# Optimization experiments

Hardware: AMD Instinct MI355X
Metric: run time of the kernel (lower is better)

The kernel has to match this reference:

```python
import jax, jax.numpy as jnp
import numpy as np
from jax import lax

H = 128  # hidden_size


def lstm_last_h(x, w_ih, w_hh, b_ih, b_hh):
    """PyTorch-style single-layer LSTM; returns final hidden state.
    x: (B, T, D). Gate order i, f, g, o. w_ih: (4H, D), w_hh: (4H, H)."""
    B = x.shape[0]
    Hh = w_hh.shape[1]
    x_proj = jnp.einsum('btd,gd->btg', x, w_ih) + b_ih + b_hh  # (B, T, 4H)

    def step(carry, xt):
        h, c = carry
        gates = xt + h @ w_hh.T
        i, f, g, o = jnp.split(gates, 4, axis=-1)
        i = jax.nn.sigmoid(i)
        f = jax.nn.sigmoid(f)
        g = jnp.tanh(g)
        o = jax.nn.sigmoid(o)
        c = f * c + i * g
        h = o * jnp.tanh(c)
        return (h, c), None

    init = (jnp.zeros((B, Hh), x.dtype), jnp.zeros((B, Hh), x.dtype))
    (h, _), _ = lax.scan(step, init, jnp.swapaxes(x_proj, 0, 1))
    return h  # (B, H)


def setup_inputs() -> dict:
    key = jax.random.key(0)
    ks = jax.random.split(key, 12)
    s = 0.05
    return {
        'x_players': jax.random.normal(ks[0], (64, 22, 128, 2), jnp.float32),
        'x_ball': jax.random.normal(ks[1], (64, 128, 2), jnp.float32),
        'p_w_ih': jax.random.normal(ks[2], (4 * H, 2), jnp.float32) * s,
        'p_w_hh': jax.random.normal(ks[3], (4 * H, H), jnp.float32) * s,
        'p_b_ih': jax.random.normal(ks[4], (4 * H,), jnp.float32) * s,
        'p_b_hh': jax.random.normal(ks[5], (4 * H,), jnp.float32) * s,
        'b_w_ih': jax.random.normal(ks[6], (4 * H, 2), jnp.float32) * s,
        'b_w_hh': jax.random.normal(ks[7], (4 * H, H), jnp.float32) * s,
        'b_b_ih': jax.random.normal(ks[8], (4 * H,), jnp.float32) * s,
        'b_b_hh': jax.random.normal(ks[9], (4 * H,), jnp.float32) * s,
        'fc_w': jax.random.normal(ks[10], (40, 2 * H), jnp.float32) * s,
        'fc_b': jax.random.normal(ks[11], (40,), jnp.float32) * s,
    }


def reference(x_players, x_ball, p_w_ih, p_w_hh, p_b_ih, p_b_hh,
              b_w_ih, b_w_hh, b_b_ih, b_b_hh, fc_w, fc_b):
    B, P, T, D = x_players.shape
    ball_h = lstm_last_h(x_ball, b_w_ih, b_w_hh, b_b_ih, b_b_hh)  # (B, H)
    # Shared player LSTM: fold players into batch (replaces per-player loop).
    ph = lstm_last_h(x_players.reshape(B * P, T, D),
                     p_w_ih, p_w_hh, p_b_ih, p_b_hh).reshape(B, P, H)
    ball_rep = jnp.broadcast_to(ball_h[:, None, :], (B, P, H))
    combined = jnp.concatenate([ph, ball_rep], axis=-1)  # (B, P, 2H)
    out = combined @ fc_w.T + fc_b  # (B, P, 40)
    return out.reshape(B, P, 20, 2)
```

## Files before the change

kernel.cpp:

```cpp
#include <hip/hip_runtime.h>


#define HDIM 128
#define TSTEPS 128
#define NPLAYER 1408
#define NSEQ 1472
#define NB 8
#define NBLK (NSEQ / NB)
#define NPBLK (NPLAYER / NB)
#define KT 5
#define BSTR 168
#define XSTR 258

typedef _Float16 f16x8 __attribute__((ext_vector_type(8)));
typedef _Float16 f16x2 __attribute__((ext_vector_type(2)));
typedef float    f32x4 __attribute__((ext_vector_type(4)));

#define LOG2E 1.44269504f

__device__ __forceinline__ float rcp_fast(float x) { return __builtin_amdgcn_rcpf(x); }
__device__ __forceinline__ float sigmoid_f(float x) {
    return rcp_fast(1.0f + __builtin_amdgcn_exp2f(-LOG2E * x));
}
__device__ __forceinline__ float tanh_f(float x) {
    return 1.0f - 2.0f * rcp_fast(__builtin_amdgcn_exp2f(2.0f * LOG2E * x) + 1.0f);
}
__device__ __forceinline__ float dpp_xor8(float x) {
    return __int_as_float(__builtin_amdgcn_update_dpp(
        __float_as_int(x), __float_as_int(x), 0x128 , 0xF, 0xF, false));
}

__global__ void __launch_bounds__(512)
__attribute__((amdgpu_waves_per_eu(2, 2)))
lstm_kernel(const float* __restrict__ x_players, const float* __restrict__ x_ball,
            const float* __restrict__ p_w_ih, const float* __restrict__ p_w_hh,
            const float* __restrict__ p_b_ih, const float* __restrict__ p_b_hh,
            const float* __restrict__ b_w_ih, const float* __restrict__ b_w_hh,
            const float* __restrict__ b_b_ih, const float* __restrict__ b_b_hh,
            float* __restrict__ h_all)
{
    const int tid  = threadIdx.x;
    const int blk  = blockIdx.x;
    const int w    = tid >> 6;
    const int lane = tid & 63;
    const int nn   = lane & 15;
    const int q    = lane >> 4;

    const bool ball = (blk >= NPBLK);
    const float* w_ih = ball ? b_w_ih : p_w_ih;
    const float* w_hh = ball ? b_w_hh : p_w_hh;
    const float* bih  = ball ? b_b_ih : p_b_ih;
    const float* bhh  = ball ? b_b_hh : p_b_hh;
    const float* xg   = ball ? (x_ball    + (size_t)(blk - NPBLK) * NB * TSTEPS * 2)
                             : (x_players + (size_t)blk * NB * TSTEPS * 2);

    __shared__ __align__(16) _Float16 b_sh[2][NB * BSTR];
    __shared__ __align__(16) float x_sh[NB * XSTR];

    for (int i = tid; i < NB * 256; i += 512)
        x_sh[(i >> 8) * XSTR + (i & 255)] = xg[i];
    for (int i = tid; i < 2 * NB * BSTR / 2; i += 512)
        ((int*)b_sh)[i] = 0;

    f16x8 afr[4][KT];
    #pragma unroll
    for (int mi = 0; mi < 4; ++mi) {
        const int r = mi * HDIM + w * 16 + nn;
        const float* wr = w_hh + (size_t)r * HDIM;
        #pragma unroll
        for (int kt = 0; kt < 4; ++kt) {
            const float* p = wr + kt * 32 + q * 8;
            f16x8 a8;
            #pragma unroll
            for (int j = 0; j < 8; ++j) a8[j] = (_Float16)p[j];
            afr[mi][kt] = a8;
        }
        f16x8 a8 = {};
        if (q == 0) {
            a8[0] = (_Float16)w_ih[2 * r];
            a8[1] = (_Float16)w_ih[2 * r + 1];
            a8[2] = (_Float16)(bih[r] + bhh[r]);
        }
        afr[mi][4] = a8;
    }

    const int colh   = nn & 7;
    const int rowoff = (nn < 8) ? 0 : 2;
    const int hrow   = w * 16 + 4 * q + rowoff;
    float c0 = 0.f, c1 = 0.f;
    float h0 = 0.f, h1 = 0.f;

    __syncthreads();
    if (tid < NB) {
        _Float16* br0 = &b_sh[0][tid * BSTR];
        br0[128] = (_Float16)x_sh[tid * XSTR];
        br0[129] = (_Float16)x_sh[tid * XSTR + 1];
        br0[130] = (_Float16)1.0f;
        b_sh[1][tid * BSTR + 130] = (_Float16)1.0f;
    }
    __syncthreads();

    f16x8 bfr[KT] = {};

    auto substep = [&](int s, const _Float16* bc, _Float16* bn, bool last) {
        if (nn < 8) {
            #pragma unroll
            for (int kt = 0; kt < KT; ++kt)
                bfr[kt] = *(const f16x8*)(bc + nn * BSTR + kt * 32 + q * 8);
        }

        f32x4 acc[4];
        #pragma unroll
        for (int mi = 0; mi < 4; ++mi) acc[mi] = (f32x4){0.f, 0.f, 0.f, 0.f};
        #pragma unroll
        for (int kt = 0; kt < KT; ++kt)
            #pragma unroll
            for (int mi = 0; mi < 4; ++mi)
                acc[mi] = __builtin_amdgcn_mfma_f32_16x16x32_f16(afr[mi][kt], bfr[kt], acc[mi], 0, 0, 0);

        if (!last && tid < NB) {
            const float x0 = x_sh[tid * XSTR + 2 * (s + 1)];
            const float x1 = x_sh[tid * XSTR + 2 * (s + 1) + 1];
            *(f16x2*)&bn[tid * BSTR + 128] = (f16x2){(_Float16)x0, (_Float16)x1};
        }

        float u0[4], u1[4];
        #pragma unroll
        for (int mi = 0; mi < 4; ++mi) {
            const float r2 = dpp_xor8(acc[mi][2]);
            const float r3 = dpp_xor8(acc[mi][3]);
            u0[mi] = (nn < 8) ? acc[mi][0] : r2;
            u1[mi] = (nn < 8) ? acc[mi][1] : r3;
        }
        const float i0 = sigmoid_f(u0[0]), i1 = sigmoid_f(u1[0]);
        const float f0 = sigmoid_f(u0[1]), f1 = sigmoid_f(u1[1]);
        const float g0 = tanh_f(u0[2]),    g1 = tanh_f(u1[2]);
        const float o0 = sigmoid_f(u0[3]), o1 = sigmoid_f(u1[3]);
        c0 = __builtin_fmaf(f0, c0, i0 * g0);
        c1 = __builtin_fmaf(f1, c1, i1 * g1);
        h0 = o0 * tanh_f(c0);
        h1 = o1 * tanh_f(c1);

        if (!last) {
            *(f16x2*)&bn[colh * BSTR + hrow] = (f16x2){(_Float16)h0, (_Float16)h1};
            __syncthreads();
        }
    };

    _Float16* b0 = &b_sh[0][0];
    _Float16* b1 = &b_sh[1][0];
    #pragma unroll 1
    for (int it = 0; it < TSTEPS / 2 - 1; ++it) {
        substep(2 * it,     b0, b1, false);
        substep(2 * it + 1, b1, b0, false);
        asm volatile("" :
            "+a"(afr[0][0]), "+a"(afr[0][1]), "+a"(afr[0][2]), "+a"(afr[0][3]), "+a"(afr[0][4]),
            "+a"(afr[1][0]), "+a"(afr[1][1]), "+a"(afr[1][2]), "+a"(afr[1][3]), "+a"(afr[1][4]),
            "+a"(afr[2][0]), "+a"(afr[2][1]), "+a"(afr[2][2]), "+a"(afr[2][3]), "+a"(afr[2][4]),
            "+a"(afr[3][0]), "+a"(afr[3][1]), "+a"(afr[3][2]), "+a"(afr[3][3]), "+a"(afr[3][4]));
    }
    substep(126, b0, b1, false);
    substep(127, b1, b0, true);

    float* hp = h_all + (size_t)(blk * NB + colh) * HDIM + hrow;
    hp[0] = h0; hp[1] = h1;
}

__global__ void __launch_bounds__(256)
fc_kernel(const float* __restrict__ h_all, const float* __restrict__ fc_w,
          const float* __restrict__ fc_b, float* __restrict__ out)
{
    const int blk = blockIdx.x;
    const int tid = threadIdx.x;

    __shared__ __align__(16) float comb[8][2 * HDIM];
    for (int i = tid; i < 8 * HDIM; i += 256) {
        const int p = i >> 7, off = i & 127;
        const int gp = 8 * blk + p;
        comb[p][off]        = h_all[(size_t)gp * HDIM + off];
        comb[p][HDIM + off] = h_all[(size_t)(NPLAYER + gp / 22) * HDIM + off];
    }
    __syncthreads();

    for (int o = tid; o < 8 * 40; o += 256) {
        const int p = o / 40, row = o - p * 40;
        const float* wr = fc_w + (size_t)row * 2 * HDIM;
        const float* cp = &comb[p][0];
        float a0 = fc_b[row], a1 = 0.f, a2 = 0.f, a3 = 0.f;
        #pragma unroll
        for (int k = 0; k < 2 * HDIM; k += 4) {
            float4 wv = *(const float4*)(wr + k);
            float4 cv = *(const float4*)(cp + k);
            a0 = __builtin_fmaf(wv.x, cv.x, a0);
            a1 = __builtin_fmaf(wv.y, cv.y, a1);
            a2 = __builtin_fmaf(wv.z, cv.z, a2);
            a3 = __builtin_fmaf(wv.w, cv.w, a3);
        }
        out[(size_t)(8 * blk + p) * 40 + row] = (a0 + a1) + (a2 + a3);
    }
}

extern "C" void kernel_launch(void* const* d_in, const int* in_sizes, int n_in,
                              void* d_out, int out_size, void* d_ws, size_t ws_size,
                              hipStream_t stream) {
    const float* x_players = (const float*)d_in[0];
    const float* x_ball    = (const float*)d_in[1];
    const float* p_w_ih    = (const float*)d_in[2];
    const float* p_w_hh    = (const float*)d_in[3];
    const float* p_b_ih    = (const float*)d_in[4];
    const float* p_b_hh    = (const float*)d_in[5];
    const float* b_w_ih    = (const float*)d_in[6];
    const float* b_w_hh    = (const float*)d_in[7];
    const float* b_b_ih    = (const float*)d_in[8];
    const float* b_b_hh    = (const float*)d_in[9];
    const float* fc_w      = (const float*)d_in[10];
    const float* fc_b      = (const float*)d_in[11];

    float* h_all = (float*)d_ws;

    lstm_kernel<<<dim3(NBLK), dim3(512), 0, stream>>>(
        x_players, x_ball, p_w_ih, p_w_hh, p_b_ih, p_b_hh,
        b_w_ih, b_w_hh, b_b_ih, b_b_hh, h_all);

    fc_kernel<<<dim3(NPBLK), dim3(256), 0, stream>>>(
        h_all, fc_w, fc_b, (float*)d_out);
}
```

Before: 185.4 us.

## Halve LSTM sequences per block and use 4-wave blocks covering 32 hidden rows each

Each block now handles 4 sequences with 256 threads instead of 8 with 512, so there are twice as many blocks (368) to fill the GPU's compute units. Each wave now owns 32 hidden rows (8 MFMA tiles) and recombines gate outputs with an extra ds_swizzle xor-4 exchange. The bias/input tile is issued first against a zero accumulator rather than zero-initializing. This doubles weight register footprint per wave and wastes more of the MFMA's 16 columns (only 4 valid), but shortens per-step barrier scope and raises occupancy.

```diff
diff --git a/kernel.cpp b/kernel.cpp
--- a/kernel.cpp
+++ b/kernel.cpp
@@ -5,7 +5,7 @@
 #define TSTEPS 128
 #define NPLAYER 1408
 #define NSEQ 1472
-#define NB 8
+#define NB 4
 #define NBLK (NSEQ / NB)
 #define NPBLK (NPLAYER / NB)
 #define KT 5
@@ -27,10 +27,13 @@
 }
 __device__ __forceinline__ float dpp_xor8(float x) {
     return __int_as_float(__builtin_amdgcn_update_dpp(
-        __float_as_int(x), __float_as_int(x), 0x128 , 0xF, 0xF, false));
-}
-
-__global__ void __launch_bounds__(512)
+        __float_as_int(x), __float_as_int(x), 0x128, 0xF, 0xF, false));
+}
+__device__ __forceinline__ float swz_xor4(float x) {
+    return __int_as_float(__builtin_amdgcn_ds_swizzle(__float_as_int(x), 0x101F));
+}
+
+__global__ void __launch_bounds__(256)
 __attribute__((amdgpu_waves_per_eu(2, 2)))
 lstm_kernel(const float* __restrict__ x_players, const float* __restrict__ x_ball,
             const float* __restrict__ p_w_ih, const float* __restrict__ p_w_hh,
@@ -45,6 +48,8 @@
     const int lane = tid & 63;
     const int nn   = lane & 15;
     const int q    = lane >> 4;
+    const int bit2 = (nn >> 2) & 1;
+    const int bit3 = (nn >> 3) & 1;
 
     const bool ball = (blk >= NPBLK);
     const float* w_ih = ball ? b_w_ih : p_w_ih;
@@ -57,38 +62,42 @@
     __shared__ __align__(16) _Float16 b_sh[2][NB * BSTR];
     __shared__ __align__(16) float x_sh[NB * XSTR];
 
-    for (int i = tid; i < NB * 256; i += 512)
+    for (int i = tid; i < NB * 256; i += 256)
         x_sh[(i >> 8) * XSTR + (i & 255)] = xg[i];
-    for (int i = tid; i < 2 * NB * BSTR / 2; i += 512)
+    for (int i = tid; i < 2 * NB * BSTR / 2; i += 256)
         ((int*)b_sh)[i] = 0;
 
-    f16x8 afr[4][KT];
+    f16x8 afr[8][KT];
     #pragma unroll
-    for (int mi = 0; mi < 4; ++mi) {
-        const int r = mi * HDIM + w * 16 + nn;
-        const float* wr = w_hh + (size_t)r * HDIM;
-        #pragma unroll
-        for (int kt = 0; kt < 4; ++kt) {
-            const float* p = wr + kt * 32 + q * 8;
-            f16x8 a8;
+    for (int g = 0; g < 4; ++g)
+        #pragma unroll
+        for (int hh = 0; hh < 2; ++hh) {
+            const int mi = 2 * g + hh;
+            const int r  = g * HDIM + w * 32 + hh * 16 + nn;
+            const float* wr = w_hh + (size_t)r * HDIM;
             #pragma unroll
-            for (int j = 0; j < 8; ++j) a8[j] = (_Float16)p[j];
-            afr[mi][kt] = a8;
-        }
-        f16x8 a8 = {};
-        if (q == 0) {
-            a8[0] = (_Float16)w_ih[2 * r];
-            a8[1] = (_Float16)w_ih[2 * r + 1];
-            a8[2] = (_Float16)(bih[r] + bhh[r]);
-        }
-        afr[mi][4] = a8;
-    }
-
-    const int colh   = nn & 7;
-    const int rowoff = (nn < 8) ? 0 : 2;
-    const int hrow   = w * 16 + 4 * q + rowoff;
-    float c0 = 0.f, c1 = 0.f;
-    float h0 = 0.f, h1 = 0.f;
+            for (int kt = 0; kt < 4; ++kt) {
+                const float* p = wr + kt * 32 + q * 8;
+                f16x8 a8;
+                #pragma unroll
+                for (int j = 0; j < 8; ++j) a8[j] = (_Float16)p[j];
+                afr[mi][kt] = a8;
+            }
+            f16x8 a8 = {};
+            if (q == 0) {
+                a8[0] = (_Float16)w_ih[2 * r];
+                a8[1] = (_Float16)w_ih[2 * r + 1];
+                a8[2] = (_Float16)(bih[r] + bhh[r]);
+            }
+            afr[mi][4] = a8;
+        }
+
+    const int colh = nn & 3;
+    const int r0   = w * 32 + bit2 * 16 + q * 4 + bit3 * 2;
+    float c0 = 0.f, c1 = 0.f, h0 = 0.f, h1 = 0.f;
+
+    f32x4 zero4 = (f32x4){0.f, 0.f, 0.f, 0.f};
+    asm volatile("" : "+v"(zero4));
 
     __syncthreads();
     if (tid < NB) {
@@ -103,19 +112,20 @@
     f16x8 bfr[KT] = {};
 
     auto substep = [&](int s, const _Float16* bc, _Float16* bn, bool last) {
-        if (nn < 8) {
+        if (nn < NB) {
             #pragma unroll
             for (int kt = 0; kt < KT; ++kt)
                 bfr[kt] = *(const f16x8*)(bc + nn * BSTR + kt * 32 + q * 8);
         }
 
-        f32x4 acc[4];
-        #pragma unroll
-        for (int mi = 0; mi < 4; ++mi) acc[mi] = (f32x4){0.f, 0.f, 0.f, 0.f};
-        #pragma unroll
-        for (int kt = 0; kt < KT; ++kt)
+        f32x4 acc[8];
+        #pragma unroll
+        for (int mi = 0; mi < 8; ++mi)
+            acc[mi] = __builtin_amdgcn_mfma_f32_16x16x32_f16(afr[mi][4], bfr[4], zero4, 0, 0, 0);
+        #pragma unroll
+        for (int kt = 0; kt < 4; ++kt)
             #pragma unroll
-            for (int mi = 0; mi < 4; ++mi)
+            for (int mi = 0; mi < 8; ++mi)
                 acc[mi] = __builtin_amdgcn_mfma_f32_16x16x32_f16(afr[mi][kt], bfr[kt], acc[mi], 0, 0, 0);
 
         if (!last && tid < NB) {
@@ -124,25 +134,34 @@
             *(f16x2*)&bn[tid * BSTR + 128] = (f16x2){(_Float16)x0, (_Float16)x1};
         }
 
-        float u0[4], u1[4];
-        #pragma unroll
-        for (int mi = 0; mi < 4; ++mi) {
+        float u[8][2];
+        #pragma unroll
+        for (int mi = 0; mi < 8; ++mi) {
             const float r2 = dpp_xor8(acc[mi][2]);
             const float r3 = dpp_xor8(acc[mi][3]);
-            u0[mi] = (nn < 8) ? acc[mi][0] : r2;
-            u1[mi] = (nn < 8) ? acc[mi][1] : r3;
-        }
-        const float i0 = sigmoid_f(u0[0]), i1 = sigmoid_f(u1[0]);
-        const float f0 = sigmoid_f(u0[1]), f1 = sigmoid_f(u1[1]);
-        const float g0 = tanh_f(u0[2]),    g1 = tanh_f(u1[2]);
-        const float o0 = sigmoid_f(u0[3]), o1 = sigmoid_f(u1[3]);
+            u[mi][0] = bit3 ? r2 : acc[mi][0];
+            u[mi][1] = bit3 ? r3 : acc[mi][1];
+        }
+        float v[4][2];
+        #pragma unroll
+        for (int g = 0; g < 4; ++g) {
+            const float p0 = swz_xor4(u[2 * g + 1][0]);
+            const float p1 = swz_xor4(u[2 * g + 1][1]);
+            v[g][0] = bit2 ? p0 : u[2 * g][0];
+            v[g][1] = bit2 ? p1 : u[2 * g][1];
+        }
+
+        const float i0 = sigmoid_f(v[0][0]), i1 = sigmoid_f(v[0][1]);
+        const float f0 = sigmoid_f(v[1][0]), f1 = sigmoid_f(v[1][1]);
+        const float g0 = tanh_f(v[2][0]),    g1 = tanh_f(v[2][1]);
+        const float o0 = sigmoid_f(v[3][0]), o1 = sigmoid_f(v[3][1]);
         c0 = __builtin_fmaf(f0, c0, i0 * g0);
         c1 = __builtin_fmaf(f1, c1, i1 * g1);
         h0 = o0 * tanh_f(c0);
         h1 = o1 * tanh_f(c1);
 
         if (!last) {
-            *(f16x2*)&bn[colh * BSTR + hrow] = (f16x2){(_Float16)h0, (_Float16)h1};
+            *(f16x2*)&bn[colh * BSTR + r0] = (f16x2){(_Float16)h0, (_Float16)h1};
             __syncthreads();
         }
     };
@@ -153,16 +172,20 @@
     for (int it = 0; it < TSTEPS / 2 - 1; ++it) {
         substep(2 * it,     b0, b1, false);
         substep(2 * it + 1, b1, b0, false);
-        asm volatile("" :
-            "+a"(afr[0][0]), "+a"(afr[0][1]), "+a"(afr[0][2]), "+a"(afr[0][3]), "+a"(afr[0][4]),
-            "+a"(afr[1][0]), "+a"(afr[1][1]), "+a"(afr[1][2]), "+a"(afr[1][3]), "+a"(afr[1][4]),
-            "+a"(afr[2][0]), "+a"(afr[2][1]), "+a"(afr[2][2]), "+a"(afr[2][3]), "+a"(afr[2][4]),
-            "+a"(afr[3][0]), "+a"(afr[3][1]), "+a"(afr[3][2]), "+a"(afr[3][3]), "+a"(afr[3][4]));
+        asm volatile("" : "+a"(afr[0][0]), "+a"(afr[0][1]), "+a"(afr[0][2]), "+a"(afr[0][3]), "+a"(afr[0][4]));
+        asm volatile("" : "+a"(afr[1][0]), "+a"(afr[1][1]), "+a"(afr[1][2]), "+a"(afr[1][3]), "+a"(afr[1][4]));
+        asm volatile("" : "+a"(afr[2][0]), "+a"(afr[2][1]), "+a"(afr[2][2]), "+a"(afr[2][3]), "+a"(afr[2][4]));
+        asm volatile("" : "+a"(afr[3][0]), "+a"(afr[3][1]), "+a"(afr[3][2]), "+a"(afr[3][3]), "+a"(afr[3][4]));
+        asm volatile("" : "+a"(afr[4][0]), "+a"(afr[4][1]), "+a"(afr[4][2]), "+a"(afr[4][3]), "+a"(afr[4][4]));
+        asm volatile("" : "+a"(afr[5][0]), "+a"(afr[5][1]), "+a"(afr[5][2]), "+a"(afr[5][3]), "+a"(afr[5][4]));
+        asm volatile("" : "+a"(afr[6][0]), "+a"(afr[6][1]), "+a"(afr[6][2]), "+a"(afr[6][3]), "+a"(afr[6][4]));
+        asm volatile("" : "+a"(afr[7][0]), "+a"(afr[7][1]), "+a"(afr[7][2]), "+a"(afr[7][3]), "+a"(afr[7][4]));
+        asm volatile("" : "+v"(zero4));
     }
     substep(126, b0, b1, false);
     substep(127, b1, b0, true);
 
-    float* hp = h_all + (size_t)(blk * NB + colh) * HDIM + hrow;
+    float* hp = h_all + (size_t)(blk * NB + colh) * HDIM + r0;
     hp[0] = h0; hp[1] = h1;
 }
 
@@ -218,10 +241,10 @@
 
     float* h_all = (float*)d_ws;
 
-    lstm_kernel<<<dim3(NBLK), dim3(512), 0, stream>>>(
+    lstm_kernel<<<dim3(NBLK), dim3(256), 0, stream>>>(
         x_players, x_ball, p_w_ih, p_w_hh, p_b_ih, p_b_hh,
         b_w_ih, b_w_hh, b_b_ih, b_b_hh, h_all);
 
-    fc_kernel<<<dim3(NPBLK), dim3(256), 0, stream>>>(
+    fc_kernel<<<dim3(NPLAYER / 8), dim3(256), 0, stream>>>(
         h_all, fc_w, fc_b, (float*)d_out);
 }
```

Measured after the change: 297.5 us. 1.6x slower.

## Fuse FC head into LSTM kernel using atomic accumulation into zeroed output

Applied to the files above, without the earlier changes.

The separate FC kernel and the h_all workspace round trip are removed. Each LSTM block computes its share of the FC output from its final hidden states in shared memory. Player blocks add their half plus the bias, and ball blocks broadcast their half to the 22 players, both through atomicAdd into an output zeroed by hipMemsetAsync. This drops one kernel launch and the global staging, but adds a memset launch and many atomics, and makes the floating-point summation order nondeterministic.

```diff
diff --git a/kernel.cpp b/kernel.cpp
--- a/kernel.cpp
+++ b/kernel.cpp
@@ -11,6 +11,7 @@
 #define KT 5
 #define BSTR 168
 #define XSTR 258
+#define HSTR 132
 
 typedef _Float16 f16x8 __attribute__((ext_vector_type(8)));
 typedef _Float16 f16x2 __attribute__((ext_vector_type(2)));
@@ -27,17 +28,18 @@
 }
 __device__ __forceinline__ float dpp_xor8(float x) {
     return __int_as_float(__builtin_amdgcn_update_dpp(
-        __float_as_int(x), __float_as_int(x), 0x128 , 0xF, 0xF, false));
+        __float_as_int(x), __float_as_int(x), 0x128, 0xF, 0xF, false));
 }
 
 __global__ void __launch_bounds__(512)
 __attribute__((amdgpu_waves_per_eu(2, 2)))
-lstm_kernel(const float* __restrict__ x_players, const float* __restrict__ x_ball,
-            const float* __restrict__ p_w_ih, const float* __restrict__ p_w_hh,
-            const float* __restrict__ p_b_ih, const float* __restrict__ p_b_hh,
-            const float* __restrict__ b_w_ih, const float* __restrict__ b_w_hh,
-            const float* __restrict__ b_b_ih, const float* __restrict__ b_b_hh,
-            float* __restrict__ h_all)
+lstm_fc_kernel(const float* __restrict__ x_players, const float* __restrict__ x_ball,
+               const float* __restrict__ p_w_ih, const float* __restrict__ p_w_hh,
+               const float* __restrict__ p_b_ih, const float* __restrict__ p_b_hh,
+               const float* __restrict__ b_w_ih, const float* __restrict__ b_w_hh,
+               const float* __restrict__ b_b_ih, const float* __restrict__ b_b_hh,
+               const float* __restrict__ fc_w, const float* __restrict__ fc_b,
+               float* __restrict__ out)
 {
     const int tid  = threadIdx.x;
     const int blk  = blockIdx.x;
@@ -56,6 +58,8 @@
 
     __shared__ __align__(16) _Float16 b_sh[2][NB * BSTR];
     __shared__ __align__(16) float x_sh[NB * XSTR];
+    __shared__ __align__(16) float hbuf[NB * HSTR];
+    __shared__ float vout[NB * 40];
 
     for (int i = tid; i < NB * 256; i += 512)
         x_sh[(i >> 8) * XSTR + (i & 255)] = xg[i];
@@ -153,50 +157,60 @@
     for (int it = 0; it < TSTEPS / 2 - 1; ++it) {
         substep(2 * it,     b0, b1, false);
         substep(2 * it + 1, b1, b0, false);
-        asm volatile("" :
-            "+a"(afr[0][0]), "+a"(afr[0][1]), "+a"(afr[0][2]), "+a"(afr[0][3]), "+a"(afr[0][4]),
-            "+a"(afr[1][0]), "+a"(afr[1][1]), "+a"(afr[1][2]), "+a"(afr[1][3]), "+a"(afr[1][4]),
-            "+a"(afr[2][0]), "+a"(afr[2][1]), "+a"(afr[2][2]), "+a"(afr[2][3]), "+a"(afr[2][4]),
-            "+a"(afr[3][0]), "+a"(afr[3][1]), "+a"(afr[3][2]), "+a"(afr[3][3]), "+a"(afr[3][4]));
+        asm volatile("" : "+a"(afr[0][0]), "+a"(afr[0][1]), "+a"(afr[0][2]), "+a"(afr[0][3]), "+a"(afr[0][4]));
+        asm volatile("" : "+a"(afr[1][0]), "+a"(afr[1][1]), "+a"(afr[1][2]), "+a"(afr[1][3]), "+a"(afr[1][4]));
+        asm volatile("" : "+a"(afr[2][0]), "+a"(afr[2][1]), "+a"(afr[2][2]), "+a"(afr[2][3]), "+a"(afr[2][4]));
+        asm volatile("" : "+a"(afr[3][0]), "+a"(afr[3][1]), "+a"(afr[3][2]), "+a"(afr[3][3]), "+a"(afr[3][4]));
     }
     substep(126, b0, b1, false);
     substep(127, b1, b0, true);
 
-    float* hp = h_all + (size_t)(blk * NB + colh) * HDIM + hrow;
-    hp[0] = h0; hp[1] = h1;
-}
-
-__global__ void __launch_bounds__(256)
-fc_kernel(const float* __restrict__ h_all, const float* __restrict__ fc_w,
-          const float* __restrict__ fc_b, float* __restrict__ out)
-{
-    const int blk = blockIdx.x;
-    const int tid = threadIdx.x;
-
-    __shared__ __align__(16) float comb[8][2 * HDIM];
-    for (int i = tid; i < 8 * HDIM; i += 256) {
-        const int p = i >> 7, off = i & 127;
-        const int gp = 8 * blk + p;
-        comb[p][off]        = h_all[(size_t)gp * HDIM + off];
-        comb[p][HDIM + off] = h_all[(size_t)(NPLAYER + gp / 22) * HDIM + off];
-    }
+    hbuf[colh * HSTR + hrow]     = h0;
+    hbuf[colh * HSTR + hrow + 1] = h1;
     __syncthreads();
 
-    for (int o = tid; o < 8 * 40; o += 256) {
-        const int p = o / 40, row = o - p * 40;
-        const float* wr = fc_w + (size_t)row * 2 * HDIM;
-        const float* cp = &comb[p][0];
-        float a0 = fc_b[row], a1 = 0.f, a2 = 0.f, a3 = 0.f;
-        #pragma unroll
-        for (int k = 0; k < 2 * HDIM; k += 4) {
-            float4 wv = *(const float4*)(wr + k);
-            float4 cv = *(const float4*)(cp + k);
-            a0 = __builtin_fmaf(wv.x, cv.x, a0);
-            a1 = __builtin_fmaf(wv.y, cv.y, a1);
-            a2 = __builtin_fmaf(wv.z, cv.z, a2);
-            a3 = __builtin_fmaf(wv.w, cv.w, a3);
-        }
-        out[(size_t)(8 * blk + p) * 40 + row] = (a0 + a1) + (a2 + a3);
+    if (!ball) {
+        for (int o = tid; o < NB * 40; o += 512) {
+            const int j = o / 40, row = o - j * 40;
+            const float* wr = fc_w + (size_t)row * 2 * HDIM;
+            const float* hp = &hbuf[j * HSTR];
+            float a0 = fc_b[row], a1 = 0.f, a2 = 0.f, a3 = 0.f;
+            #pragma unroll
+            for (int k = 0; k < HDIM; k += 4) {
+                float4 wv = *(const float4*)(wr + k);
+                float4 hv = *(const float4*)(hp + k);
+                a0 = __builtin_fmaf(wv.x, hv.x, a0);
+                a1 = __builtin_fmaf(wv.y, hv.y, a1);
+                a2 = __builtin_fmaf(wv.z, hv.z, a2);
+                a3 = __builtin_fmaf(wv.w, hv.w, a3);
+            }
+            atomicAdd(&out[(size_t)(NB * blk + j) * 40 + row], (a0 + a1) + (a2 + a3));
+        }
+    } else {
+        for (int o = tid; o < NB * 40; o += 512) {
+            const int c = o / 40, row = o - c * 40;
+            const float* wr = fc_w + (size_t)row * 2 * HDIM + HDIM;
+            const float* hp = &hbuf[c * HSTR];
+            float a0 = 0.f, a1 = 0.f, a2 = 0.f, a3 = 0.f;
+            #pragma unroll
+            for (int k = 0; k < HDIM; k += 4) {
+                float4 wv = *(const float4*)(wr + k);
+                float4 hv = *(const float4*)(hp + k);
+                a0 = __builtin_fmaf(wv.x, hv.x, a0);
+                a1 = __builtin_fmaf(wv.y, hv.y, a1);
+                a2 = __builtin_fmaf(wv.z, hv.z, a2);
+                a3 = __builtin_fmaf(wv.w, hv.w, a3);
+            }
+            vout[c * 40 + row] = (a0 + a1) + (a2 + a3);
+        }
+        __syncthreads();
+        const int base_batch = (blk - NPBLK) * NB;
+        for (int o = tid; o < NB * 22 * 40; o += 512) {
+            const int c = o / 880, rem = o - c * 880;
+            const int p = rem / 40, row = rem - p * 40;
+            atomicAdd(&out[(size_t)((base_batch + c) * 22 + p) * 40 + row],
+                      vout[c * 40 + row]);
+        }
     }
 }
 
@@ -216,12 +230,9 @@
     const float* fc_w      = (const float*)d_in[10];
     const float* fc_b      = (const float*)d_in[11];
 
-    float* h_all = (float*)d_ws;
-
-    lstm_kernel<<<dim3(NBLK), dim3(512), 0, stream>>>(
+    hipMemsetAsync(d_out, 0, (size_t)out_size * sizeof(float), stream);
+
+    lstm_fc_kernel<<<dim3(NBLK), dim3(512), 0, stream>>>(
         x_players, x_ball, p_w_ih, p_w_hh, p_b_ih, p_b_hh,
-        b_w_ih, b_w_hh, b_b_ih, b_b_hh, h_all);
-
-    fc_kernel<<<dim3(NPBLK), dim3(256), 0, stream>>>(
-        h_all, fc_w, fc_b, (float*)d_out);
-}
+        b_w_ih, b_w_hh, b_b_ih, b_b_hh, fc_w, fc_b, (float*)d_out);
+}
```

Result: faster. 180.5 us (-2.6%).
